# Kernel optimization log

Measured on AMD Instinct MI355X. Metric: run time of the kernel, lower is better.

The kernel has to match this reference:

```python
import jax, jax.numpy as jnp
import numpy as np

B, S, D, M = 4, 8192, 1024, 512  # batch, seq_len, dim, memory_dim (= dim // 2)
LN_EPS = 1e-5


def _layernorm(z, g, b):
    mu = jnp.mean(z, axis=-1, keepdims=True)
    var = jnp.var(z, axis=-1, keepdims=True)
    return (z - mu) * jax.lax.rsqrt(var + LN_EPS) * g + b


def setup_inputs() -> dict:
    key = jax.random.key(0)
    ks = jax.random.split(key, 16)
    s_d = 1.0 / np.sqrt(D)
    s_m = 1.0 / np.sqrt(M)
    return {
        "x": jax.random.normal(ks[0], (B, S, D), jnp.float32),
        "Wd": jax.random.normal(ks[1], (D, M), jnp.float32) * s_d,
        "bd": jnp.zeros((M,), jnp.float32),
        "Wq": jax.random.normal(ks[2], (M, M), jnp.float32) * s_m,
        "bq": jnp.zeros((M,), jnp.float32),
        "Wk": jax.random.normal(ks[3], (M, M), jnp.float32) * s_m,
        "bk": jnp.zeros((M,), jnp.float32),
        "Wv": jax.random.normal(ks[4], (M, M), jnp.float32) * s_m,
        "bv": jnp.zeros((M,), jnp.float32),
        "gq": jnp.ones((M,), jnp.float32),
        "bq_ln": jnp.zeros((M,), jnp.float32),
        "gk": jnp.ones((M,), jnp.float32),
        "bk_ln": jnp.zeros((M,), jnp.float32),
        "W1": jax.random.normal(ks[5], (M, M), jnp.float32) * s_m,  # MemoryMLP layer 1
        "W2": jax.random.normal(ks[6], (M, M), jnp.float32) * s_m,  # MemoryMLP layer 2
        "Wu": jax.random.normal(ks[7], (M, D), jnp.float32) * s_m,
        "bu": jnp.zeros((D,), jnp.float32),
        "adaptive_lr": jnp.float32(0.01),
        "forget_factor": jnp.float32(0.1),
    }


def reference(x, Wd, bd, Wq, bq, Wk, bk, Wv, bv, gq, bq_ln, gk, bk_ln,
              W1, W2, Wu, bu, adaptive_lr, forget_factor):
    # project to memory dim: [B,S,M]
    h = jnp.einsum('bsd,dm->bsm', x, Wd) + bd
    q = _layernorm(h @ Wq + bq, gq, bq_ln)
    k = _layernorm(h @ Wk + bk, gk, bk_ln)
    v = h @ Wv + bv
    # MemoryMLP prediction on keys (depth 2, gelu between)
    pred = jax.nn.gelu(k @ W1) @ W2
    # surprise (negative gradient direction of MSE store loss), lr-scaled
    u = adaptive_lr * (v - pred)                       # inputs to scan [B,S,M]
    g = jax.nn.sigmoid(forget_factor)                  # scalar retention gate
    gates = jnp.full((B, S, 1), g, dtype=x.dtype)
    # gated linear recurrence s_t = g_t * s_{t-1} + u_t  (AssocScan math)
    def combine(a, c):
        g1, u1 = a
        g2, u2 = c
        return (g1 * g2, u1 * g2 + u2)
    _, mem = jax.lax.associative_scan(combine, (gates, u), axis=1)  # [B,S,M]
    # query-gated readout, project up, residual ('mal' integration)
    retrieved = q * mem
    out = x + jnp.einsum('bsm,md->bsd', retrieved, Wu) + bu
    return out
```

## Files before the change

### kernel.cpp

```cpp
#include <hip/hip_runtime.h>
#include <hip/hip_bf16.h>
#include <cstdint>


typedef unsigned short u16;
typedef unsigned int u32;
typedef __attribute__((ext_vector_type(8))) short short8;
typedef __attribute__((ext_vector_type(4))) float f32x4;

#define R_ROWS 32768
#define S_LEN 8192
#define D_DIM 1024
#define M_DIM 512

__device__ __forceinline__ float bf2f(u16 u) {
  union { unsigned int i; float f; } v; v.i = ((unsigned int)u) << 16; return v.f;
}
__device__ __forceinline__ u16 f2bf(float f) {
  union { float f; unsigned int i; } v; v.f = f;
  unsigned int r = v.i + 0x7fff + ((v.i >> 16) & 1);
  return (u16)(r >> 16);
}

__global__ __launch_bounds__(256)
void prep_all(const float* __restrict__ x, u16* __restrict__ xb,
              const float* __restrict__ Wd, const float* __restrict__ Wq,
              const float* __restrict__ Wk, const float* __restrict__ Wv,
              const float* __restrict__ W1, const float* __restrict__ W2,
              const float* __restrict__ Wu, const float* __restrict__ bq,
              const float* __restrict__ bk, const float* __restrict__ bv,
              u16* __restrict__ WdT, u16* __restrict__ WqkvT,
              u16* __restrict__ W1T, u16* __restrict__ W2T,
              u16* __restrict__ WuT, float* __restrict__ bqkv) {
  __shared__ u16 tile[32][33];
  int id = blockIdx.x;
  if (id >= 2310) {
    const long i = ((long)(id - 2310) * 256 + threadIdx.x) * 8;
    short8 o;
#pragma unroll
    for (int j = 0; j < 8; ++j) o[j] = (short)f2bf(x[i + j]);
    *(short8*)(xb + i) = o;
    return;
  }
  if (id >= 2304) {
    const int i = (id - 2304) * 256 + threadIdx.x;
    bqkv[i] = (i < 512) ? bq[i] : (i < 1024) ? bk[i - 512] : bv[i - 1024];
    return;
  }
  const float* src;
  u16* dst;
  int rows, cols, bx, by;
  if (id < 512) {
    src = Wd; dst = WdT; rows = 1024; cols = 512;
    bx = id & 15; by = id >> 4;
  } else if (id < 768) {
    src = Wq; dst = WqkvT; rows = 512; cols = 512;
    id -= 512; bx = id & 15; by = id >> 4;
  } else if (id < 1024) {
    src = Wk; dst = WqkvT + 512 * 512; rows = 512; cols = 512;
    id -= 768; bx = id & 15; by = id >> 4;
  } else if (id < 1280) {
    src = Wv; dst = WqkvT + 2 * 512 * 512; rows = 512; cols = 512;
    id -= 1024; bx = id & 15; by = id >> 4;
  } else if (id < 1536) {
    src = W1; dst = W1T; rows = 512; cols = 512;
    id -= 1280; bx = id & 15; by = id >> 4;
  } else if (id < 1792) {
    src = W2; dst = W2T; rows = 512; cols = 512;
    id -= 1536; bx = id & 15; by = id >> 4;
  } else {
    src = Wu; dst = WuT; rows = 512; cols = 1024;
    id -= 1792; bx = id & 31; by = id >> 5;
  }
  const int tx = threadIdx.x & 31;
  const int ty = threadIdx.x >> 5;
  const int c = bx * 32 + tx;
#pragma unroll
  for (int i = 0; i < 32; i += 8)
    tile[ty + i][tx] = f2bf(src[(long)(by * 32 + ty + i) * cols + c]);
  __syncthreads();
  const int c2 = by * 32 + tx;
#pragma unroll
  for (int i = 0; i < 32; i += 8)
    dst[(long)(bx * 32 + ty + i) * rows + c2] = tile[tx][ty + i];
}


#define BARRIER()                          \
  __builtin_amdgcn_sched_barrier(0);       \
  __builtin_amdgcn_s_barrier();            \
  __builtin_amdgcn_sched_barrier(0)

#define RD_A(D, QM, AF)                                                     \
  _Pragma("unroll") for (int mi = 0; mi < 4; ++mi)                          \
  _Pragma("unroll") for (int kk = 0; kk < 2; ++kk)                          \
    AF[mi][kk] = *(const short8*)(smem + (D) * 65536 +                      \
        (wm * 128 + (QM) * 64 + mi * 16 + l15) * 128 +                      \
        ((kk * 64 + lg * 16) ^ xre));

#define RD_B(D, QN, BF)                                                     \
  _Pragma("unroll") for (int j = 0; j < 2; ++j)                             \
  _Pragma("unroll") for (int kk = 0; kk < 2; ++kk)                          \
    BF[j][kk] = *(const short8*)(smem + (D) * 65536 + 32768 +               \
        (wn * 64 + (QN) * 32 + j * 16 + l15) * 128 +                        \
        ((kk * 64 + lg * 16) ^ xre));

#define DO_MFMA(QM, QN, AF, BF)                                             \
  __builtin_amdgcn_s_setprio(1);                                            \
  _Pragma("unroll") for (int mi = 0; mi < 4; ++mi)                          \
  _Pragma("unroll") for (int j = 0; j < 2; ++j)                             \
  _Pragma("unroll") for (int kk = 0; kk < 2; ++kk)                          \
    acc[(QM) * 4 + mi][(QN) * 2 + j] =                                      \
        __builtin_amdgcn_mfma_f32_16x16x32_bf16(                            \
            AF[mi][kk], BF[j][kk], acc[(QM) * 4 + mi][(QN) * 2 + j], 0, 0, 0); \
  __builtin_amdgcn_s_setprio(0)

template <int EPI>
__global__ __launch_bounds__(512, 1)
void gemm8p(const u16* __restrict__ A, const u16* __restrict__ BT,
            const float* __restrict__ bias, void* __restrict__ Cv,
            const int K, const int N,
            const void* __restrict__ auxv, const float* __restrict__ sclr) {
  __shared__ __align__(16) char smem[131072];
  const int tid = threadIdx.x;
  const int lane = tid & 63;
  const int wid = tid >> 6;
  const int l15 = lane & 15;
  const int lg = lane >> 4;
  const int wm = wid >> 2;
  const int wn = wid & 3;
  const long am0 = (long)blockIdx.x * 256;
  const long bn0 = (long)blockIdx.y * 256;
  const int s_r = lane >> 3;
  const int s_c = ((lane & 7) << 3) ^ ((lane >> 3) << 3);
  const int xre = (l15 & 7) << 4;

  f32x4 acc[8][4];
#pragma unroll
  for (int i = 0; i < 8; ++i)
#pragma unroll
    for (int j = 0; j < 4; ++j) acc[i][j] = (f32x4){0.f, 0.f, 0.f, 0.f};

  const int NT = K >> 6;
  const int NITER = NT >> 1;

  auto stg = [&](int d, int arr, int half, int kt) {
    const int k0 = kt << 6;
    const u16* src = arr ? BT : A;
    const long rb0 = arr ? bn0 : am0;
    char* base = smem + d * 65536 + arr * 32768 + half * 16384;
#pragma unroll
    for (int i = 0; i < 2; ++i) {
      const int jr = (wid * 2 + i) * 8;
      const u16* g =
          src + (rb0 + half * 128 + jr + s_r) * (long)K + (k0 + s_c);
      __builtin_amdgcn_global_load_lds(
          (const __attribute__((address_space(1))) void*)g,
          (__attribute__((address_space(3))) void*)(base + jr * 128), 16, 0, 0);
    }
  };

  stg(0, 1, 0, 0); stg(0, 1, 1, 0);
  stg(0, 0, 0, 0); stg(0, 0, 1, 0);
  stg(1, 1, 0, 1); stg(1, 1, 1, 1);
  asm volatile("s_waitcnt vmcnt(4)" ::: "memory");
  BARRIER();

  short8 aF[4][2], bF0[2][2], bF1[2][2];
#pragma unroll 1
  for (int t = 0; t < NITER; ++t) {
    const int kt1 = 2 * t + 1;
    const int kt2 = (2 * t + 2 < NT) ? 2 * t + 2 : NT - 1;
    const int kt3 = (2 * t + 3 < NT) ? 2 * t + 3 : NT - 1;
    RD_A(0, 0, aF); RD_B(0, 0, bF0);
    stg(1, 0, 0, kt1);
    BARRIER();
    DO_MFMA(0, 0, aF, bF0);
    BARRIER();
    RD_B(0, 1, bF1);
    stg(1, 0, 1, kt1);
    BARRIER();
    DO_MFMA(0, 1, aF, bF1);
    BARRIER();
    RD_A(0, 1, aF);
    stg(0, 1, 0, kt2);
    BARRIER();
    DO_MFMA(1, 1, aF, bF1);
    BARRIER();
    stg(0, 1, 1, kt2);
    BARRIER();
    DO_MFMA(1, 0, aF, bF0);
    asm volatile("s_waitcnt vmcnt(4)" ::: "memory");
    BARRIER();
    RD_A(1, 0, aF); RD_B(1, 0, bF0);
    stg(0, 0, 0, kt2);
    BARRIER();
    DO_MFMA(0, 0, aF, bF0);
    BARRIER();
    RD_B(1, 1, bF1);
    stg(0, 0, 1, kt2);
    BARRIER();
    DO_MFMA(0, 1, aF, bF1);
    BARRIER();
    RD_A(1, 1, aF);
    stg(1, 1, 0, kt3);
    BARRIER();
    DO_MFMA(1, 1, aF, bF1);
    BARRIER();
    stg(1, 1, 1, kt3);
    BARRIER();
    DO_MFMA(1, 0, aF, bF0);
    asm volatile("s_waitcnt vmcnt(4)" ::: "memory");
    BARRIER();
  }

  if constexpr (EPI == 3) {
    float* Cs = (float*)smem;
    const u16* xb = (const u16*)auxv;
    float* Of = (float*)Cv;
    const int tseg = (tid & 63) * 4;
    const int trw = tid >> 6;
#pragma unroll
    for (int p = 0; p < 8; ++p) {
      __syncthreads();
      if (wm == (p >> 2)) {
        const int mbase = (p & 3) * 2;
#pragma unroll
        for (int mm = 0; mm < 2; ++mm)
#pragma unroll
          for (int ni = 0; ni < 4; ++ni)
#pragma unroll
            for (int r = 0; r < 4; ++r)
              Cs[(mm * 16 + lg * 4 + r) * 260 + wn * 64 + ni * 16 + l15] =
                  acc[mbase + mm][ni][r];
      }
      __syncthreads();
#pragma unroll
      for (int rb = 0; rb < 32; rb += 8) {
        const int lrow = rb + trw;
        const long row = am0 + p * 32 + lrow;
        const long col = bn0 + tseg;
        f32x4 cv = *(const f32x4*)&Cs[lrow * 260 + tseg];
        const u32* xp = (const u32*)(xb + row * N + col);
        const u32 x0 = xp[0], x1 = xp[1];
        const f32x4 bv = *(const f32x4*)&bias[col];
        cv[0] += bf2f((u16)(x0 & 0xffff)) + bv[0];
        cv[1] += bf2f((u16)(x0 >> 16)) + bv[1];
        cv[2] += bf2f((u16)(x1 & 0xffff)) + bv[2];
        cv[3] += bf2f((u16)(x1 >> 16)) + bv[3];
        *(f32x4*)&Of[row * N + col] = cv;
      }
    }
    return;
  }

  float lr = 0.f;
  if (EPI == 2) lr = *sclr;
#pragma unroll
  for (int mi = 0; mi < 8; ++mi) {
    const long row0 = am0 + wm * 128 + mi * 16 + lg * 4;
#pragma unroll
    for (int ni = 0; ni < 4; ++ni) {
      const long col = bn0 + wn * 64 + ni * 16 + l15;
      const float bb = bias ? bias[col] : 0.f;
#pragma unroll
      for (int r = 0; r < 4; ++r) {
        const long row = row0 + r;
        float c = acc[mi][ni][r] + bb;
        if (EPI == 1) {
          c = 0.5f * c * (1.f + tanhf(0.7978845608028654f * (c + 0.044715f * c * c * c)));
        } else if (EPI == 2) {
          c = lr * (bf2f(((const u16*)auxv)[row * N + col]) - c);
        }
        if (EPI == 4) {
          const long sel = col >> 9;
          ((u16*)Cv)[sel * ((long)R_ROWS * M_DIM) + row * M_DIM + (col & 511)] =
              f2bf(c);
        } else {
          ((u16*)Cv)[row * N + col] = f2bf(c);
        }
      }
    }
  }
}

__global__ __launch_bounds__(256)
void ln_qk(u16* __restrict__ q, u16* __restrict__ k,
           const float* __restrict__ gq, const float* __restrict__ bq,
           const float* __restrict__ gk, const float* __restrict__ bk) {
  const int wid = threadIdx.x >> 6, lane = threadIdx.x & 63;
  long job = (long)blockIdx.x * 4 + wid;
  u16* base;
  const float *g, *b;
  if (job < R_ROWS) { base = q; g = gq; b = bq; }
  else { base = k; g = gk; b = bk; job -= R_ROWS; }
  u16* p = base + job * M_DIM + lane * 8;
  short8 zv = *(short8*)p;
  float z[8], s = 0.f, s2 = 0.f;
#pragma unroll
  for (int i = 0; i < 8; ++i) {
    z[i] = bf2f((u16)zv[i]);
    s += z[i];
    s2 += z[i] * z[i];
  }
#pragma unroll
  for (int off = 32; off >= 1; off >>= 1) {
    s += __shfl_xor(s, off);
    s2 += __shfl_xor(s2, off);
  }
  const float mu = s * (1.f / 512.f);
  const float inv = rsqrtf(s2 * (1.f / 512.f) - mu * mu + 1e-5f);
#pragma unroll
  for (int i = 0; i < 8; ++i) {
    float y = (z[i] - mu) * inv * g[lane * 8 + i] + b[lane * 8 + i];
    zv[i] = (short)f2bf(y);
  }
  *(short8*)p = zv;
}

#define SCAN_CH 32
#define SCAN_L (S_LEN / SCAN_CH)
#define SCAN_W 64

__global__ __launch_bounds__(256)
void scan_mul(const u16* __restrict__ u, const u16* __restrict__ q,
              u16* __restrict__ retr, const float* __restrict__ ffp) {
  const int m2 = threadIdx.x;
  const int b = blockIdx.x / SCAN_CH;
  const int ch = blockIdx.x % SCAN_CH;
  const float g = 1.f / (1.f + __expf(-*ffp));
  const long base = ((long)b * S_LEN) * M_DIM + 2 * m2;
  const int t0 = ch * SCAN_L;
  const int tw = (t0 >= SCAN_W) ? (t0 - SCAN_W) : 0;
  float s0 = 0.f, s1 = 0.f;
#pragma unroll 8
  for (int t = tw; t < t0; ++t) {
    const u32 w = *(const u32*)(u + base + (long)t * M_DIM);
    s0 = g * s0 + bf2f((u16)(w & 0xffff));
    s1 = g * s1 + bf2f((u16)(w >> 16));
  }
#pragma unroll 8
  for (int t = t0; t < t0 + SCAN_L; ++t) {
    const long idx = base + (long)t * M_DIM;
    const u32 w = *(const u32*)(u + idx);
    s0 = g * s0 + bf2f((u16)(w & 0xffff));
    s1 = g * s1 + bf2f((u16)(w >> 16));
    const u32 qw = *(const u32*)(q + idx);
    const u32 o = (u32)f2bf(bf2f((u16)(qw & 0xffff)) * s0) |
                  ((u32)f2bf(bf2f((u16)(qw >> 16)) * s1) << 16);
    *(u32*)(retr + idx) = o;
  }
}

extern "C" void kernel_launch(void* const* d_in, const int* in_sizes, int n_in,
                              void* d_out, int out_size, void* d_ws,
                              size_t ws_size, hipStream_t stream) {
  const float* x = (const float*)d_in[0];
  const float* Wd = (const float*)d_in[1];
  const float* bd = (const float*)d_in[2];
  const float* Wq = (const float*)d_in[3];
  const float* bq = (const float*)d_in[4];
  const float* Wk = (const float*)d_in[5];
  const float* bk = (const float*)d_in[6];
  const float* Wv = (const float*)d_in[7];
  const float* bv = (const float*)d_in[8];
  const float* gq = (const float*)d_in[9];
  const float* bq_ln = (const float*)d_in[10];
  const float* gk = (const float*)d_in[11];
  const float* bk_ln = (const float*)d_in[12];
  const float* W1 = (const float*)d_in[13];
  const float* W2 = (const float*)d_in[14];
  const float* Wu = (const float*)d_in[15];
  const float* bu = (const float*)d_in[16];
  const float* lr = (const float*)d_in[17];
  const float* ff = (const float*)d_in[18];

  char* w = (char*)d_ws;
  auto alloc = [&](size_t bytes) {
    char* p = w;
    w += (bytes + 255) & ~(size_t)255;
    return (u16*)p;
  };
  u16* WdT = alloc(512 * 1024 * 2);
  u16* WqkvT = alloc((size_t)1536 * 512 * 2);
  u16* W1T = alloc(512 * 512 * 2);
  u16* W2T = alloc(512 * 512 * 2);
  u16* WuT = alloc(1024 * 512 * 2);
  float* bqkv = (float*)alloc(1536 * 4);
  const size_t act = (size_t)R_ROWS * M_DIM * 2;
  u16* xb = alloc(2 * act);
  u16* hB = alloc(act);
  u16* qB = alloc(act);
  u16* kB = alloc(act);
  u16* vB = alloc(act);
  u16* t1 = hB;
  u16* uB = kB;
  u16* retr = vB;

  dim3 tb(256);
  prep_all<<<dim3(2310 + 16384), tb, 0, stream>>>(
      x, xb, Wd, Wq, Wk, Wv, W1, W2, Wu, bq, bk, bv,
      WdT, WqkvT, W1T, W2T, WuT, bqkv);

  gemm8p<0><<<dim3(128, 2), 512, 0, stream>>>(xb, WdT, bd, hB, 1024, 512, nullptr, nullptr);
  gemm8p<4><<<dim3(128, 6), 512, 0, stream>>>(hB, WqkvT, bqkv, qB, 512, 512, nullptr, nullptr);
  ln_qk<<<dim3(16384), 256, 0, stream>>>(qB, kB, gq, bq_ln, gk, bk_ln);
  gemm8p<1><<<dim3(128, 2), 512, 0, stream>>>(kB, W1T, nullptr, t1, 512, 512, nullptr, nullptr);
  gemm8p<2><<<dim3(128, 2), 512, 0, stream>>>(t1, W2T, nullptr, uB, 512, 512, vB, lr);
  scan_mul<<<dim3(4 * SCAN_CH), 256, 0, stream>>>(uB, qB, retr, ff);
  gemm8p<3><<<dim3(128, 4), 512, 0, stream>>>(retr, WuT, bu, d_out, 512, 1024, xb, nullptr);
}
```

Before: 338.4 us.

## Fold LayerNorm into W1 GEMM epilogue and scan, keep only row stats

Replaces the in-place LayerNorm pass over q and k with a stats-only kernel that writes per-row mean and inverse std. The k-normalisation is folded algebraically into the W1 GEMM: gk scales W1's rows during prep, precomputed column sums of gk·W1 and bk_ln·W1 correct the result, and the GELU epilogue applies the per-row stats. The q-normalisation is applied on the fly inside scan_mul. This removes the write-back of two large bf16 activation tensors, at the cost of feeding un-normalised bf16 k into the matmul, which may lose precision, and of a serial 512-iteration loop in prep.

```diff
diff --git a/kernel.cpp b/kernel.cpp
--- a/kernel.cpp
+++ b/kernel.cpp
@@ -29,17 +29,31 @@
               const float* __restrict__ W1, const float* __restrict__ W2,
               const float* __restrict__ Wu, const float* __restrict__ bq,
               const float* __restrict__ bk, const float* __restrict__ bv,
+              const float* __restrict__ gk, const float* __restrict__ bk_ln,
               u16* __restrict__ WdT, u16* __restrict__ WqkvT,
               u16* __restrict__ W1T, u16* __restrict__ W2T,
-              u16* __restrict__ WuT, float* __restrict__ bqkv) {
+              u16* __restrict__ WuT, float* __restrict__ bqkv,
+              float* __restrict__ G, float* __restrict__ Bv) {
   __shared__ u16 tile[32][33];
   int id = blockIdx.x;
-  if (id >= 2310) {
-    const long i = ((long)(id - 2310) * 256 + threadIdx.x) * 8;
+  if (id >= 2312) {
+    const long i = ((long)(id - 2312) * 256 + threadIdx.x) * 8;
     short8 o;
 #pragma unroll
     for (int j = 0; j < 8; ++j) o[j] = (short)f2bf(x[i + j]);
     *(short8*)(xb + i) = o;
+    return;
+  }
+  if (id >= 2310) {
+    const int j = (id - 2310) * 256 + threadIdx.x;
+    float sG = 0.f, sB = 0.f;
+    for (int c = 0; c < 512; ++c) {
+      const float w = W1[c * 512 + j];
+      sG += gk[c] * w;
+      sB += bk_ln[c] * w;
+    }
+    G[j] = sG;
+    Bv[j] = sB;
     return;
   }
   if (id >= 2304) {
@@ -50,6 +64,7 @@
   const float* src;
   u16* dst;
   int rows, cols, bx, by;
+  bool foldg = false;
   if (id < 512) {
     src = Wd; dst = WdT; rows = 1024; cols = 512;
     bx = id & 15; by = id >> 4;
@@ -65,6 +80,7 @@
   } else if (id < 1536) {
     src = W1; dst = W1T; rows = 512; cols = 512;
     id -= 1280; bx = id & 15; by = id >> 4;
+    foldg = true;
   } else if (id < 1792) {
     src = W2; dst = W2T; rows = 512; cols = 512;
     id -= 1536; bx = id & 15; by = id >> 4;
@@ -76,13 +92,44 @@
   const int ty = threadIdx.x >> 5;
   const int c = bx * 32 + tx;
 #pragma unroll
-  for (int i = 0; i < 32; i += 8)
-    tile[ty + i][tx] = f2bf(src[(long)(by * 32 + ty + i) * cols + c]);
+  for (int i = 0; i < 32; i += 8) {
+    const int r = by * 32 + ty + i;
+    float v = src[(long)r * cols + c];
+    if (foldg) v *= gk[r];
+    tile[ty + i][tx] = f2bf(v);
+  }
   __syncthreads();
   const int c2 = by * 32 + tx;
 #pragma unroll
   for (int i = 0; i < 32; i += 8)
     dst[(long)(bx * 32 + ty + i) * rows + c2] = tile[tx][ty + i];
+}
+
+__global__ __launch_bounds__(256)
+void ln_stats(const u16* __restrict__ q, const u16* __restrict__ k,
+              float2* __restrict__ statq, float2* __restrict__ statk) {
+  const int wid = threadIdx.x >> 6, lane = threadIdx.x & 63;
+  long job = (long)blockIdx.x * 4 + wid;
+  const u16* base;
+  float2* outp;
+  if (job < R_ROWS) { base = q + job * M_DIM; outp = statq + job; }
+  else { base = k + (job - R_ROWS) * M_DIM; outp = statk + (job - R_ROWS); }
+  short8 zv = *(const short8*)(base + lane * 8);
+  float s = 0.f, s2 = 0.f;
+#pragma unroll
+  for (int i = 0; i < 8; ++i) {
+    const float z = bf2f((u16)zv[i]);
+    s += z;
+    s2 += z * z;
+  }
+#pragma unroll
+  for (int off = 32; off >= 1; off >>= 1) {
+    s += __shfl_xor(s, off);
+    s2 += __shfl_xor(s2, off);
+  }
+  const float mu = s * (1.f / 512.f);
+  const float inv = rsqrtf(s2 * (1.f / 512.f) - mu * mu + 1e-5f);
+  if (lane == 0) *outp = make_float2(mu, inv);
 }
 
 
@@ -254,6 +301,36 @@
     return;
   }
 
+  if constexpr (EPI == 5) {
+    const float2* stk = (const float2*)auxv;
+    const float* Gf = bias;
+    const float* Bf = sclr;
+    u16* C = (u16*)Cv;
+#pragma unroll
+    for (int mi = 0; mi < 8; ++mi) {
+      const long row0 = am0 + wm * 128 + mi * 16 + lg * 4;
+      float a_[4], b_[4];
+#pragma unroll
+      for (int r = 0; r < 4; ++r) {
+        const float2 st = stk[row0 + r];
+        a_[r] = st.y;
+        b_[r] = st.y * st.x;
+      }
+#pragma unroll
+      for (int ni = 0; ni < 4; ++ni) {
+        const long col = bn0 + wn * 64 + ni * 16 + l15;
+        const float Gc = Gf[col], Bc = Bf[col];
+#pragma unroll
+        for (int r = 0; r < 4; ++r) {
+          float c = a_[r] * acc[mi][ni][r] - b_[r] * Gc + Bc;
+          c = 0.5f * c * (1.f + tanhf(0.7978845608028654f * (c + 0.044715f * c * c * c)));
+          C[(row0 + r) * N + col] = f2bf(c);
+        }
+      }
+    }
+    return;
+  }
+
   float lr = 0.f;
   if (EPI == 2) lr = *sclr;
 #pragma unroll
@@ -267,9 +344,7 @@
       for (int r = 0; r < 4; ++r) {
         const long row = row0 + r;
         float c = acc[mi][ni][r] + bb;
-        if (EPI == 1) {
-          c = 0.5f * c * (1.f + tanhf(0.7978845608028654f * (c + 0.044715f * c * c * c)));
-        } else if (EPI == 2) {
+        if (EPI == 2) {
           c = lr * (bf2f(((const u16*)auxv)[row * N + col]) - c);
         }
         if (EPI == 4) {
@@ -284,52 +359,24 @@
   }
 }
 
-__global__ __launch_bounds__(256)
-void ln_qk(u16* __restrict__ q, u16* __restrict__ k,
-           const float* __restrict__ gq, const float* __restrict__ bq,
-           const float* __restrict__ gk, const float* __restrict__ bk) {
-  const int wid = threadIdx.x >> 6, lane = threadIdx.x & 63;
-  long job = (long)blockIdx.x * 4 + wid;
-  u16* base;
-  const float *g, *b;
-  if (job < R_ROWS) { base = q; g = gq; b = bq; }
-  else { base = k; g = gk; b = bk; job -= R_ROWS; }
-  u16* p = base + job * M_DIM + lane * 8;
-  short8 zv = *(short8*)p;
-  float z[8], s = 0.f, s2 = 0.f;
-#pragma unroll
-  for (int i = 0; i < 8; ++i) {
-    z[i] = bf2f((u16)zv[i]);
-    s += z[i];
-    s2 += z[i] * z[i];
-  }
-#pragma unroll
-  for (int off = 32; off >= 1; off >>= 1) {
-    s += __shfl_xor(s, off);
-    s2 += __shfl_xor(s2, off);
-  }
-  const float mu = s * (1.f / 512.f);
-  const float inv = rsqrtf(s2 * (1.f / 512.f) - mu * mu + 1e-5f);
-#pragma unroll
-  for (int i = 0; i < 8; ++i) {
-    float y = (z[i] - mu) * inv * g[lane * 8 + i] + b[lane * 8 + i];
-    zv[i] = (short)f2bf(y);
-  }
-  *(short8*)p = zv;
-}
-
 #define SCAN_CH 32
 #define SCAN_L (S_LEN / SCAN_CH)
 #define SCAN_W 64
 
 __global__ __launch_bounds__(256)
 void scan_mul(const u16* __restrict__ u, const u16* __restrict__ q,
-              u16* __restrict__ retr, const float* __restrict__ ffp) {
+              u16* __restrict__ retr, const float* __restrict__ ffp,
+              const float2* __restrict__ statq, const float* __restrict__ gq,
+              const float* __restrict__ bq_ln) {
   const int m2 = threadIdx.x;
   const int b = blockIdx.x / SCAN_CH;
   const int ch = blockIdx.x % SCAN_CH;
   const float g = 1.f / (1.f + __expf(-*ffp));
-  const long base = ((long)b * S_LEN) * M_DIM + 2 * m2;
+  const int c0 = 2 * m2;
+  const float g0 = gq[c0], g1 = gq[c0 + 1];
+  const float b0 = bq_ln[c0], b1 = bq_ln[c0 + 1];
+  const long rbase = (long)b * S_LEN;
+  const long base = rbase * M_DIM + c0;
   const int t0 = ch * SCAN_L;
   const int tw = (t0 >= SCAN_W) ? (t0 - SCAN_W) : 0;
   float s0 = 0.f, s1 = 0.f;
@@ -339,15 +386,17 @@
     s0 = g * s0 + bf2f((u16)(w & 0xffff));
     s1 = g * s1 + bf2f((u16)(w >> 16));
   }
-#pragma unroll 8
+#pragma unroll 4
   for (int t = t0; t < t0 + SCAN_L; ++t) {
     const long idx = base + (long)t * M_DIM;
     const u32 w = *(const u32*)(u + idx);
     s0 = g * s0 + bf2f((u16)(w & 0xffff));
     s1 = g * s1 + bf2f((u16)(w >> 16));
     const u32 qw = *(const u32*)(q + idx);
-    const u32 o = (u32)f2bf(bf2f((u16)(qw & 0xffff)) * s0) |
-                  ((u32)f2bf(bf2f((u16)(qw >> 16)) * s1) << 16);
+    const float2 st = statq[rbase + t];
+    const float q0 = (bf2f((u16)(qw & 0xffff)) - st.x) * st.y * g0 + b0;
+    const float q1 = (bf2f((u16)(qw >> 16)) - st.x) * st.y * g1 + b1;
+    const u32 o = (u32)f2bf(q0 * s0) | ((u32)f2bf(q1 * s1) << 16);
     *(u32*)(retr + idx) = o;
   }
 }
@@ -387,6 +436,10 @@
   u16* W2T = alloc(512 * 512 * 2);
   u16* WuT = alloc(1024 * 512 * 2);
   float* bqkv = (float*)alloc(1536 * 4);
+  float* Gv = (float*)alloc(512 * 4);
+  float* Bvv = (float*)alloc(512 * 4);
+  float2* statq = (float2*)alloc((size_t)R_ROWS * 8);
+  float2* statk = (float2*)alloc((size_t)R_ROWS * 8);
   const size_t act = (size_t)R_ROWS * M_DIM * 2;
   u16* xb = alloc(2 * act);
   u16* hB = alloc(act);
@@ -398,15 +451,15 @@
   u16* retr = vB;
 
   dim3 tb(256);
-  prep_all<<<dim3(2310 + 16384), tb, 0, stream>>>(
-      x, xb, Wd, Wq, Wk, Wv, W1, W2, Wu, bq, bk, bv,
-      WdT, WqkvT, W1T, W2T, WuT, bqkv);
+  prep_all<<<dim3(2312 + 16384), tb, 0, stream>>>(
+      x, xb, Wd, Wq, Wk, Wv, W1, W2, Wu, bq, bk, bv, gk, bk_ln,
+      WdT, WqkvT, W1T, W2T, WuT, bqkv, Gv, Bvv);
 
   gemm8p<0><<<dim3(128, 2), 512, 0, stream>>>(xb, WdT, bd, hB, 1024, 512, nullptr, nullptr);
   gemm8p<4><<<dim3(128, 6), 512, 0, stream>>>(hB, WqkvT, bqkv, qB, 512, 512, nullptr, nullptr);
-  ln_qk<<<dim3(16384), 256, 0, stream>>>(qB, kB, gq, bq_ln, gk, bk_ln);
-  gemm8p<1><<<dim3(128, 2), 512, 0, stream>>>(kB, W1T, nullptr, t1, 512, 512, nullptr, nullptr);
+  ln_stats<<<dim3(16384), tb, 0, stream>>>(qB, kB, statq, statk);
+  gemm8p<5><<<dim3(128, 2), 512, 0, stream>>>(kB, W1T, Gv, t1, 512, 512, statk, Bvv);
   gemm8p<2><<<dim3(128, 2), 512, 0, stream>>>(t1, W2T, nullptr, uB, 512, 512, vB, lr);
-  scan_mul<<<dim3(4 * SCAN_CH), 256, 0, stream>>>(uB, qB, retr, ff);
+  scan_mul<<<dim3(4 * SCAN_CH), tb, 0, stream>>>(uB, qB, retr, ff, statq, gq, bq_ln);
   gemm8p<3><<<dim3(128, 4), 512, 0, stream>>>(retr, WuT, bu, d_out, 512, 1024, xb, nullptr);
 }
```

Measured after the change: 358.3 us. 1.06x slower.
